# Kernel tuning notes

Measured on AMD Instinct MI355X. Metric: run time of the kernel, lower is better.

The kernel has to match this reference:

```python
import jax, jax.numpy as jnp
import numpy as np

B, N, H = 32, 1024, 512
THR = 0.05  # peak_detection_threshold


def _l2norm(x):
    return x / jnp.linalg.norm(x, axis=-1, keepdims=True)


def setup_inputs() -> dict:
    key = jax.random.key(0)
    ks = jax.random.split(key, 6)
    def w(k, shape, fan_in):
        return jax.random.normal(k, shape, jnp.float32) / np.float32(np.sqrt(fan_in))
    return {
        "segment_rep": jax.random.normal(ks[0], (B, N, H), jnp.float32),
        "phn_mask": jnp.ones((B, N), jnp.float32),
        # SegmentSimilarityMeasure: Linear(2H->H), ReLU, Linear(H->1, no bias)
        "W1": w(ks[1], (2 * H, H), 2 * H),
        "b1": jnp.zeros((H,), jnp.float32),
        "W2": w(ks[2], (H, 1), H),
        # word_enc: Linear(H->H), ReLU, Linear(H->H)
        "We1": w(ks[3], (H, H), H),
        "be1": jnp.zeros((H,), jnp.float32),
        "We2": w(ks[4], (H, H), H),
        "be2": jnp.zeros((H,), jnp.float32),
    }


def _forward(segment_rep, phn_mask, W1, b1, W2, We1, be1, We2, be2):
    Bs, Np, Hd = segment_rep.shape
    # adjacent segment similarity: MLP on concat of l2-normalized neighbors -> (B, N-1)
    cat = jnp.concatenate([_l2norm(segment_rep[:, :-1, :]), _l2norm(segment_rep[:, 1:, :])], axis=2)
    S = (jax.nn.relu(cat @ W1 + b1) @ W2)[..., 0]

    # relative dissimilarity
    Smin = jnp.min(S, axis=1, keepdims=True)
    Smax = jnp.max(S, axis=1, keepdims=True)
    D = 1.0 - (S - Smin) / (Smax - Smin)

    # peak detector (faithful to original, incl. final overwrite of first-order cols -2:)
    z = jnp.zeros_like(D)
    fo = z
    fo = fo.at[:, 0].set(jnp.maximum(D[:, 0] - D[:, 1], 0.0))
    fo = fo.at[:, 1:-1].set(jnp.minimum(jnp.maximum(D[:, 1:-1] - D[:, :-2], 0.0),
                                        jnp.maximum(D[:, 1:-1] - D[:, 2:], 0.0)))
    fo = fo.at[:, -1].set(jnp.maximum(D[:, -1] - D[:, -2], 0.0))
    so = z
    so = so.at[:, 0:2].set(jnp.maximum(D[:, 0:2] - D[:, 2:4], 0.0))
    so = so.at[:, 2:-2].set(jnp.minimum(jnp.maximum(D[:, 2:-2] - D[:, :-4], 0.0),
                                        jnp.maximum(D[:, 2:-2] - D[:, 4:], 0.0)))
    fo = fo.at[:, -2:].set(jnp.maximum(D[:, -2:] - D[:, -4:-2], 0.0))  # replicates original code
    P = jnp.minimum(jnp.maximum(jnp.maximum(fo, so) - THR, 0.0), fo)

    # pad, mask, straight-through hard boundaries
    P = jnp.pad(P, ((0, 0), (0, 1)))
    P = jax.nn.relu(P + (phn_mask - 1.0))
    b_soft = jnp.tanh(10.0 * P)
    b_hard = jnp.tanh(100000.0 * P)
    b = b_soft + jax.lax.stop_gradient(b_hard - b_soft)
    b = jnp.cumsum(b, axis=1)  # (B, N)
    b = b + (b[:, :1] == 0).astype(b.dtype)  # per-row +1 if b[:,0]==0
    num_word_segments = b[:, -1].astype(jnp.int32) + 1  # (B,)

    # U: column j holds j+1 for j < num_word_segments[i], else -100000. Nmax = N (static bound).
    cols = jnp.arange(1, Np + 1, dtype=jnp.int32)  # (Nmax,)
    U = jnp.where(cols[None, :] <= num_word_segments[:, None],
                  cols.astype(segment_rep.dtype)[None, :], -100000.0)  # (B, Nmax)

    V = U[:, None, :] - b[:, :, None]  # (B, N, Nmax)
    Wseg = 1.0 - jnp.tanh(100000.0 * jnp.abs(V))
    Wseg = Wseg / jnp.sum(Wseg, axis=1, keepdims=True)
    Wseg = jnp.nan_to_num(Wseg)

    # pool: (B, Nmax, N) @ (B, N, H) -> (B, Nmax, H)
    word_rep = jnp.einsum('bnm,bnh->bmh', Wseg, segment_rep)
    word_masks = jnp.where(word_rep == 0, 0.0, 1.0)
    out = jax.nn.relu(word_rep @ We1 + be1) @ We2 + be2
    return out * word_masks


def reference(segment_rep, phn_mask, W1, b1, W2, We1, be1, We2, be2):
    return _forward(segment_rep, phn_mask, W1, b1, W2, We1, be1, We2, be2)
```

## Files before the change

kernel.cpp:

```cpp
#include <hip/hip_runtime.h>

#define BB 32
#define NN 1024
#define HH 512
#define NS 1023

typedef unsigned short u16;
typedef unsigned int   u32;
typedef __attribute__((ext_vector_type(8))) short bf16x8;
typedef __attribute__((ext_vector_type(4))) float f32x4;

__device__ __forceinline__ float bf2f(u16 h) {
  union { u32 u; float f; } c; c.u = ((u32)h) << 16; return c.f;
}
__device__ __forceinline__ u16 f2bf(float f) {
  union { float f; u32 u; } c; c.f = f;
  u32 u = c.u;
  return (u16)((u + 0x7fffu + ((u >> 16) & 1u)) >> 16);
}
__device__ __forceinline__ void split_bf(float x, u16& hi, u16& lo) {
  hi = f2bf(x);
  lo = f2bf(x - bf2f(hi));
}
__device__ __forceinline__ void dma16(const u16* g, u16* l) {
  __builtin_amdgcn_global_load_lds(
      (const __attribute__((address_space(1))) u32*)g,
      (__attribute__((address_space(3))) u32*)l, 16, 0, 0);
}

__global__ __launch_bounds__(64) void k_prep_a(const float* __restrict__ seg,
                                               u16* __restrict__ ahi,
                                               u16* __restrict__ alo) {
  int row = blockIdx.x, lane = threadIdx.x;
  const float4* p = (const float4*)(seg + ((size_t)row << 9) + lane * 8);
  float4 a = p[0], b = p[1];
  float v[8] = {a.x, a.y, a.z, a.w, b.x, b.y, b.z, b.w};
  float s = 0.f;
#pragma unroll
  for (int i = 0; i < 8; ++i) s += v[i] * v[i];
#pragma unroll
  for (int m = 32; m; m >>= 1) s += __shfl_xor(s, m, 64);
  float nrm = sqrtf(s);
  u16 h[8], l[8];
#pragma unroll
  for (int i = 0; i < 8; ++i) split_bf(v[i] / nrm, h[i], l[i]);
  size_t off = ((size_t)row << 9) + lane * 8;
  *(uint4*)(ahi + off) = make_uint4(h[0] | (h[1] << 16), h[2] | (h[3] << 16),
                                    h[4] | (h[5] << 16), h[6] | (h[7] << 16));
  *(uint4*)(alo + off) = make_uint4(l[0] | (l[1] << 16), l[2] | (l[3] << 16),
                                    l[4] | (l[5] << 16), l[6] | (l[7] << 16));
}

__global__ __launch_bounds__(256) void k_tr(const float* __restrict__ src,
                                            u16* __restrict__ dh,
                                            u16* __restrict__ dl,
                                            int K, int N) {
  __shared__ u16 Th[64 * 66], Tl[64 * 66];
  int nb = blockIdx.x * 64, kb = blockIdx.y * 64;
  int tid = threadIdx.x;
#pragma unroll
  for (int i = 0; i < 16; ++i) {
    int e = tid + i * 256;
    int r = e >> 6, c = e & 63;
    float v = src[(size_t)(kb + r) * N + nb + c];
    u16 hi, lo; split_bf(v, hi, lo);
    Th[c * 66 + r] = hi;
    Tl[c * 66 + r] = lo;
  }
  __syncthreads();
#pragma unroll
  for (int i = 0; i < 16; ++i) {
    int e = tid + i * 256;
    int n = e >> 6, k = e & 63;
    dh[(size_t)(nb + n) * K + kb + k] = Th[n * 66 + k];
    if (dl) dl[(size_t)(nb + n) * K + kb + k] = Tl[n * 66 + k];
  }
}

__global__ __launch_bounds__(512, 2) void k_sgemm(const u16* __restrict__ ahi,
                                                  const u16* __restrict__ alo,
                                                  const u16* __restrict__ w1h,
                                                  const u16* __restrict__ w1l,
                                                  const float* __restrict__ b1,
                                                  const float* __restrict__ W2,
                                                  float* __restrict__ Spart) {
  __shared__ u16 Ah[2][256 * 32];
  __shared__ u16 Al[2][256 * 32];
  __shared__ u16 Bh[2][256 * 32];
  __shared__ u16 Bl[2][256 * 32];

  const int tid  = threadIdx.x;
  const int wave = tid >> 6, lane = tid & 63;
  const int quad = lane >> 4, l15 = lane & 15;
  const int wm = wave >> 2, wn = wave & 3;
  const int r_in = lane >> 2, c_in = lane & 3;
  const int nblk = blockIdx.x, mblk = blockIdx.y;
  const int mrow0 = mblk * 256;
  const int ncol0 = nblk * 256;

#define SG_A(g_, tb_, ks_)                                                   \
  {                                                                          \
    int k0_ = (ks_) * 32, half_ = k0_ >> 9, cb_ = k0_ & 511;                 \
    int grow_ = mrow0 + wave * 32 + (g_) * 16 + r_in + half_;                \
    if (grow_ > 32767) grow_ = 32767;                                        \
    size_t ga_ = (((size_t)grow_) << 9) + cb_ + c_in * 8;                    \
    dma16(ahi + ga_, &Ah[tb_][(wave * 32 + (g_) * 16) * 32]);                \
    dma16(alo + ga_, &Al[tb_][(wave * 32 + (g_) * 16) * 32]);                \
  }
#define SG_B(g_, tb_, ks_)                                                   \
  {                                                                          \
    int k0_ = (ks_) * 32;                                                    \
    int n_ = ncol0 + wave * 32 + (g_) * 16 + r_in;                           \
    size_t gb_ = (((size_t)n_) << 10) + k0_ + c_in * 8;                      \
    dma16(w1h + gb_, &Bh[tb_][(wave * 32 + (g_) * 16) * 32]);                \
    dma16(w1l + gb_, &Bl[tb_][(wave * 32 + (g_) * 16) * 32]);                \
  }

  f32x4 acc[8][4];
#pragma unroll
  for (int mi = 0; mi < 8; ++mi)
#pragma unroll
    for (int ni = 0; ni < 4; ++ni) acc[mi][ni] = (f32x4){0.f, 0.f, 0.f, 0.f};

  SG_A(0, 0, 0) SG_A(1, 0, 0) SG_B(0, 0, 0) SG_B(1, 0, 0)
  asm volatile("s_waitcnt vmcnt(0)" ::: "memory");
  __builtin_amdgcn_s_barrier();

  for (int ks = 0; ks < 32; ++ks) {
    const int bb = ks & 1;
    const bool pre = (ks + 1) < 32;
    bf16x8 ah[8], al[8], bh[4], bl[4];

#pragma unroll
    for (int mi = 0; mi < 8; ++mi)
      ah[mi] = *(const bf16x8*)&Ah[bb][(wm * 128 + mi * 16 + l15) * 32 + quad * 8];
#pragma unroll
    for (int ni = 0; ni < 4; ++ni)
      bh[ni] = *(const bf16x8*)&Bh[bb][(wn * 64 + ni * 16 + l15) * 32 + quad * 8];
    if (pre) { SG_A(0, bb ^ 1, ks + 1) SG_B(0, bb ^ 1, ks + 1) }
    __builtin_amdgcn_s_barrier();
    asm volatile("s_waitcnt lgkmcnt(0)" ::: "memory");
    __builtin_amdgcn_sched_barrier(0);
    __builtin_amdgcn_s_setprio(1);
#pragma unroll
    for (int ni = 0; ni < 4; ++ni)
#pragma unroll
      for (int mi = 0; mi < 8; ++mi)
        acc[mi][ni] = __builtin_amdgcn_mfma_f32_16x16x32_bf16(ah[mi], bh[ni], acc[mi][ni], 0, 0, 0);
    __builtin_amdgcn_s_setprio(0);
    __builtin_amdgcn_s_barrier();

#pragma unroll
    for (int ni = 0; ni < 4; ++ni)
      bl[ni] = *(const bf16x8*)&Bl[bb][(wn * 64 + ni * 16 + l15) * 32 + quad * 8];
    if (pre) { SG_A(1, bb ^ 1, ks + 1) SG_B(1, bb ^ 1, ks + 1) }
    __builtin_amdgcn_s_barrier();
    asm volatile("s_waitcnt lgkmcnt(0)" ::: "memory");
    __builtin_amdgcn_sched_barrier(0);
    __builtin_amdgcn_s_setprio(1);
#pragma unroll
    for (int ni = 0; ni < 4; ++ni)
#pragma unroll
      for (int mi = 0; mi < 8; ++mi)
        acc[mi][ni] = __builtin_amdgcn_mfma_f32_16x16x32_bf16(ah[mi], bl[ni], acc[mi][ni], 0, 0, 0);
    __builtin_amdgcn_s_setprio(0);
    __builtin_amdgcn_s_barrier();

#pragma unroll
    for (int mi = 0; mi < 8; ++mi)
      al[mi] = *(const bf16x8*)&Al[bb][(wm * 128 + mi * 16 + l15) * 32 + quad * 8];
    __builtin_amdgcn_s_barrier();
    asm volatile("s_waitcnt lgkmcnt(0)" ::: "memory");
    __builtin_amdgcn_sched_barrier(0);
    __builtin_amdgcn_s_setprio(1);
#pragma unroll
    for (int ni = 0; ni < 4; ++ni)
#pragma unroll
      for (int mi = 0; mi < 8; ++mi)
        acc[mi][ni] = __builtin_amdgcn_mfma_f32_16x16x32_bf16(al[mi], bh[ni], acc[mi][ni], 0, 0, 0);
    __builtin_amdgcn_s_setprio(0);
    asm volatile("s_waitcnt vmcnt(0)" ::: "memory");
    __builtin_amdgcn_s_barrier();
  }
#undef SG_A
#undef SG_B

  float* red = (float*)&Ah[0][0];
  float b1v[4], w2v[4];
#pragma unroll
  for (int ni = 0; ni < 4; ++ni) {
    int n_g = ncol0 + wn * 64 + ni * 16 + l15;
    b1v[ni] = b1[n_g];
    w2v[ni] = W2[n_g];
  }
#pragma unroll
  for (int mi = 0; mi < 8; ++mi) {
#pragma unroll
    for (int reg = 0; reg < 4; ++reg) {
      float part = 0.f;
#pragma unroll
      for (int ni = 0; ni < 4; ++ni) {
        float h = acc[mi][ni][reg] + b1v[ni];
        h = h > 0.f ? h : 0.f;
        part = fmaf(h, w2v[ni], part);
      }
#pragma unroll
      for (int m = 8; m; m >>= 1) part += __shfl_xor(part, m, 64);
      if (l15 == 0) red[wave * 128 + mi * 16 + quad * 4 + reg] = part;
    }
  }
  __syncthreads();
  if (tid < 256) {
    int wmr = tid >> 7, rl = tid & 127;
    float s = red[(wmr * 4 + 0) * 128 + rl] + red[(wmr * 4 + 1) * 128 + rl]
            + red[(wmr * 4 + 2) * 128 + rl] + red[(wmr * 4 + 3) * 128 + rl];
    int grow = mrow0 + tid;
    int b = grow >> 10, n = grow & 1023;
    if (n < NS)
      Spart[((size_t)nblk * BB + b) * NN + n] = s;
  }
}

__global__ __launch_bounds__(256) void k_row(const float* __restrict__ S0,
                                             const float* __restrict__ S1,
                                             const float* __restrict__ mask,
                                             int* __restrict__ assign,
                                             float* __restrict__ weight,
                                             float* __restrict__ total,
                                             int* __restrict__ startn,
                                             int* __restrict__ endn) {
  int b = blockIdx.x, tid = threadIdx.x;
  __shared__ float Ssh[NS];
  __shared__ float Dsh[NS];
  __shared__ float tsh[NN];
  __shared__ float bsh[NN];
  __shared__ float totl[NN];
  __shared__ int   stl[NN];
  __shared__ int   enl[NN];
  __shared__ float red[256];

  for (int n = tid; n < NS; n += 256)
    Ssh[n] = S0[((size_t)b << 10) + n] + S1[((size_t)b << 10) + n];
  __syncthreads();

  float mn = INFINITY, mx = -INFINITY;
  for (int n = tid; n < NS; n += 256) {
    float v = Ssh[n];
    mn = fminf(mn, v); mx = fmaxf(mx, v);
  }
  red[tid] = mn; __syncthreads();
  for (int s = 128; s; s >>= 1) { if (tid < s) red[tid] = fminf(red[tid], red[tid + s]); __syncthreads(); }
  float Smin = red[0]; __syncthreads();
  red[tid] = mx; __syncthreads();
  for (int s = 128; s; s >>= 1) { if (tid < s) red[tid] = fmaxf(red[tid], red[tid + s]); __syncthreads(); }
  float Smax = red[0]; __syncthreads();

  for (int n = tid; n < NS; n += 256)
    Dsh[n] = 1.0f - (Ssh[n] - Smin) / (Smax - Smin);
  __syncthreads();

  for (int n = tid; n < NN; n += 256) {
    float P;
    if (n >= NS) {
      P = 0.f;
    } else {
      float D = Dsh[n];
      float fo, so;
      if (n == 0)            fo = fmaxf(D - Dsh[1], 0.f);
      else if (n >= NS - 2)  fo = fmaxf(D - Dsh[n - 2], 0.f);
      else                   fo = fminf(fmaxf(D - Dsh[n - 1], 0.f),
                                        fmaxf(D - Dsh[n + 1], 0.f));
      if (n <= 1)            so = fmaxf(D - Dsh[n + 2], 0.f);
      else if (n >= NS - 2)  so = 0.f;
      else                   so = fminf(fmaxf(D - Dsh[n - 2], 0.f),
                                        fmaxf(D - Dsh[n + 2], 0.f));
      P = fminf(fmaxf(fmaxf(fo, so) - 0.05f, 0.f), fo);
    }
    float m = mask[((size_t)b << 10) + n];
    P = P + (m - 1.0f);
    P = P > 0.f ? P : 0.f;
    float bs = tanhf(10.0f * P);
    float bh = tanhf(100000.0f * P);
    tsh[n] = bs + (bh - bs);
  }
  __syncthreads();

  if (tid == 0) {
    float acc = 0.f;
    for (int n = 0; n < NN; n += 8) {
      float t0 = tsh[n + 0], t1 = tsh[n + 1], t2 = tsh[n + 2], t3 = tsh[n + 3];
      float t4 = tsh[n + 4], t5 = tsh[n + 5], t6 = tsh[n + 6], t7 = tsh[n + 7];
      acc += t0; bsh[n + 0] = acc; acc += t1; bsh[n + 1] = acc;
      acc += t2; bsh[n + 2] = acc; acc += t3; bsh[n + 3] = acc;
      acc += t4; bsh[n + 4] = acc; acc += t5; bsh[n + 5] = acc;
      acc += t6; bsh[n + 6] = acc; acc += t7; bsh[n + 7] = acc;
    }
  }
  __syncthreads();

  float add1 = (bsh[0] == 0.0f) ? 1.0f : 0.0f;
  int   num  = (int)(bsh[NN - 1] + add1) + 1;

  for (int mi = tid; mi < NN; mi += 256) { totl[mi] = 0.f; stl[mi] = 1 << 30; enl[mi] = -1; }
  __syncthreads();

  for (int n = tid; n < NN; n += 256) {
    float bv = bsh[n] + add1;
    float kf = rintf(bv);
    int   k  = (int)kf;
    int   a  = -1; float w = 0.f;
    if (k >= 1 && k <= num && k <= NN) {
      float v = fabsf(kf - bv);
      w = 1.0f - tanhf(100000.0f * v);
      if (w > 0.f) {
        a = k - 1;
        atomicAdd(&totl[a], w);
        atomicMin(&stl[a], n);
        atomicMax(&enl[a], n);
      } else {
        a = -1; w = 0.f;
      }
    }
    assign[((size_t)b << 10) + n] = a;
    weight[((size_t)b << 10) + n] = w;
  }
  __syncthreads();
  for (int mi = tid; mi < NN; mi += 256) {
    total [((size_t)b << 10) + mi] = totl[mi];
    startn[((size_t)b << 10) + mi] = stl[mi];
    endn  [((size_t)b << 10) + mi] = enl[mi];
  }
}

__global__ __launch_bounds__(64) void k_pool(const float* __restrict__ seg,
                                             const int* __restrict__ assign,
                                             const float* __restrict__ weight,
                                             const float* __restrict__ total,
                                             const int* __restrict__ startn,
                                             const int* __restrict__ endn,
                                             float* __restrict__ wrep) {
  int bm = blockIdx.x;
  int b  = bm >> 10, m = bm & 1023;
  int lane = threadIdx.x;
  float acc[8] = {0.f, 0.f, 0.f, 0.f, 0.f, 0.f, 0.f, 0.f};
  float tm = total[bm];
  if (tm > 0.f) {
    int s = startn[bm], e = endn[bm];
    for (int n = s; n <= e; ++n) {
      if (assign[((size_t)b << 10) + n] != m) continue;
      float coef = weight[((size_t)b << 10) + n] / tm;
      const float4* p = (const float4*)(seg + (((size_t)b << 10) + n) * HH + lane * 8);
      float4 x = p[0], y = p[1];
      acc[0] = fmaf(coef, x.x, acc[0]); acc[1] = fmaf(coef, x.y, acc[1]);
      acc[2] = fmaf(coef, x.z, acc[2]); acc[3] = fmaf(coef, x.w, acc[3]);
      acc[4] = fmaf(coef, y.x, acc[4]); acc[5] = fmaf(coef, y.y, acc[5]);
      acc[6] = fmaf(coef, y.z, acc[6]); acc[7] = fmaf(coef, y.w, acc[7]);
    }
  }
  float4* dst = (float4*)(wrep + (size_t)bm * HH + lane * 8);
  dst[0] = make_float4(acc[0], acc[1], acc[2], acc[3]);
  dst[1] = make_float4(acc[4], acc[5], acc[6], acc[7]);
}

__global__ __launch_bounds__(512) void k_out(const u16* __restrict__ we1t,
                                             const u16* __restrict__ we2t,
                                             const float* __restrict__ be1,
                                             const float* __restrict__ be2,
                                             float* __restrict__ io) {
  __shared__ u16 Hid[64 * 520];
  __shared__ u16 Wst[2][512 * 32];
  __shared__ u16 Ast[2][64 * 32];

  int tid = threadIdx.x;
  int wave = tid >> 6, lane = tid & 63, quad = lane >> 4, l15 = lane & 15;
  int wm = wave >> 2, wn = wave & 3;
  int rowbase = blockIdx.x * 64;
  int m_st = tid >> 3, ch_st = tid & 7;
  int r_in = lane >> 2, c_in = lane & 3;

#define STAGE_W(src_, ks_, tb_)                                                     \
  {                                                                                 \
    int k0_ = (ks_) * 32;                                                           \
    _Pragma("unroll")                                                               \
    for (int c_ = 0; c_ < 4; ++c_) {                                                \
      int n_ = wave * 64 + c_ * 16 + r_in;                                          \
      dma16(src_ + (size_t)n_ * 512 + k0_ + c_in * 8,                               \
            &Wst[tb_][(wave * 64 + c_ * 16) * 32]);                                 \
    }                                                                               \
  }

  f32x4 acc[2][8];
#pragma unroll
  for (int mi = 0; mi < 2; ++mi)
#pragma unroll
    for (int ni = 0; ni < 8; ++ni) acc[mi][ni] = (f32x4){0.f, 0.f, 0.f, 0.f};

  {
    float4 v = *(const float4*)(io + (size_t)(rowbase + m_st) * HH + ch_st * 4);
    u32 p0 = f2bf(v.x) | ((u32)f2bf(v.y) << 16);
    u32 p1 = f2bf(v.z) | ((u32)f2bf(v.w) << 16);
    *(uint2*)&Ast[0][m_st * 32 + ch_st * 4] = make_uint2(p0, p1);
  }
  STAGE_W(we1t, 0, 0)
  __syncthreads();

  for (int ks = 0; ks < 16; ++ks) {
    int bb = ks & 1;
    bool have = (ks + 1) < 16;
    float4 nx;
    if (have) {
      STAGE_W(we1t, ks + 1, bb ^ 1)
      nx = *(const float4*)(io + (size_t)(rowbase + m_st) * HH + (ks + 1) * 32 + ch_st * 4);
    }
    bf16x8 a[2];
#pragma unroll
    for (int mi = 0; mi < 2; ++mi)
      a[mi] = *(const bf16x8*)&Ast[bb][(wm * 32 + mi * 16 + l15) * 32 + quad * 8];
#pragma unroll
    for (int ni = 0; ni < 8; ++ni) {
      bf16x8 bw = *(const bf16x8*)&Wst[bb][(wn * 128 + ni * 16 + l15) * 32 + quad * 8];
#pragma unroll
      for (int mi = 0; mi < 2; ++mi)
        acc[mi][ni] = __builtin_amdgcn_mfma_f32_16x16x32_bf16(a[mi], bw, acc[mi][ni], 0, 0, 0);
    }
    if (have) {
      u32 p0 = f2bf(nx.x) | ((u32)f2bf(nx.y) << 16);
      u32 p1 = f2bf(nx.z) | ((u32)f2bf(nx.w) << 16);
      *(uint2*)&Ast[bb ^ 1][m_st * 32 + ch_st * 4] = make_uint2(p0, p1);
    }
    __syncthreads();
  }
#pragma unroll
  for (int mi = 0; mi < 2; ++mi)
#pragma unroll
    for (int ni = 0; ni < 8; ++ni)
#pragma unroll
      for (int reg = 0; reg < 4; ++reg) {
        int n_g = wn * 128 + ni * 16 + l15;
        float h = acc[mi][ni][reg] + be1[n_g];
        h = h > 0.f ? h : 0.f;
        Hid[(wm * 32 + mi * 16 + quad * 4 + reg) * 520 + n_g] = f2bf(h);
      }

#pragma unroll
  for (int mi = 0; mi < 2; ++mi)
#pragma unroll
    for (int ni = 0; ni < 8; ++ni) acc[mi][ni] = (f32x4){0.f, 0.f, 0.f, 0.f};

  STAGE_W(we2t, 0, 0)
  __syncthreads();

  for (int ks = 0; ks < 16; ++ks) {
    int bb = ks & 1;
    if (ks + 1 < 16) STAGE_W(we2t, ks + 1, bb ^ 1)
    int k0 = ks * 32;
    bf16x8 a[2];
#pragma unroll
    for (int mi = 0; mi < 2; ++mi)
      a[mi] = *(const bf16x8*)&Hid[(wm * 32 + mi * 16 + l15) * 520 + k0 + quad * 8];
#pragma unroll
    for (int ni = 0; ni < 8; ++ni) {
      bf16x8 bw = *(const bf16x8*)&Wst[bb][(wn * 128 + ni * 16 + l15) * 32 + quad * 8];
#pragma unroll
      for (int mi = 0; mi < 2; ++mi)
        acc[mi][ni] = __builtin_amdgcn_mfma_f32_16x16x32_bf16(a[mi], bw, acc[mi][ni], 0, 0, 0);
    }
    __syncthreads();
  }
#undef STAGE_W

#pragma unroll
  for (int mi = 0; mi < 2; ++mi)
#pragma unroll
    for (int ni = 0; ni < 8; ++ni)
#pragma unroll
      for (int reg = 0; reg < 4; ++reg) {
        int n_g = wn * 128 + ni * 16 + l15;
        size_t row = (size_t)(rowbase + wm * 32 + mi * 16 + quad * 4 + reg);
        float o = acc[mi][ni][reg] + be2[n_g];
        float wr = io[row * HH + n_g];
        io[row * HH + n_g] = (wr == 0.f) ? 0.f : o;
      }
}

__global__ void k_diag(float* __restrict__ out, int hostcode) {
  if (hostcode != 0) out[0] = (float)hostcode;
}

extern "C" void kernel_launch(void* const* d_in, const int* in_sizes, int n_in,
                              void* d_out, int out_size, void* d_ws, size_t ws_size,
                              hipStream_t stream) {
  const float* seg  = (const float*)d_in[0];
  const float* mask = (const float*)d_in[1];
  const float* W1   = (const float*)d_in[2];
  const float* b1   = (const float*)d_in[3];
  const float* W2   = (const float*)d_in[4];
  const float* We1  = (const float*)d_in[5];
  const float* be1  = (const float*)d_in[6];
  const float* We2  = (const float*)d_in[7];
  const float* be2  = (const float*)d_in[8];

  const size_t NROW = (size_t)BB * NN;
  float* ws = (float*)d_ws;
  float* S0     = ws;
  float* S1     = S0 + NROW;
  int*   assign = (int*)(S1 + NROW);
  float* weight = (float*)(assign + NROW);
  float* total  = weight + NROW;
  int*   startn = (int*)(total + NROW);
  int*   endn   = startn + NROW;
  u16*   w1h    = (u16*)(endn + NROW);
  u16*   w1l    = w1h + (size_t)512 * 1024;
  u16*   we1t   = w1l + (size_t)512 * 1024;
  u16*   we2t   = we1t + (size_t)512 * 512;

  float* out = (float*)d_out;
  u16*   ahi = (u16*)d_out;
  u16*   alo = ahi + (size_t)NROW * HH;

  int hostcode = 0;
  if (ws_size < (size_t)7 * NROW * 4 + (size_t)3 * 1024 * 1024) hostcode += 32768;
  if (out_size != 16777216) hostcode += 8192;

  k_prep_a<<<dim3(BB * NN), dim3(64), 0, stream>>>(seg, ahi, alo);
  k_tr    <<<dim3(8, 16), dim3(256), 0, stream>>>(W1, w1h, w1l, 1024, 512);
  k_tr    <<<dim3(8, 8),  dim3(256), 0, stream>>>(We1, we1t, (u16*)nullptr, 512, 512);
  k_tr    <<<dim3(8, 8),  dim3(256), 0, stream>>>(We2, we2t, (u16*)nullptr, 512, 512);
  k_sgemm <<<dim3(2, 128), dim3(512), 0, stream>>>(ahi, alo, w1h, w1l, b1, W2, S0);
  k_row   <<<dim3(BB), dim3(256), 0, stream>>>(S0, S1, mask, assign, weight, total, startn, endn);
  k_pool  <<<dim3(BB * NN), dim3(64), 0, stream>>>(seg, assign, weight, total, startn, endn, out);
  k_out   <<<dim3(NROW / 64), dim3(512), 0, stream>>>(we1t, we2t, be1, be2, out);
  k_diag  <<<dim3(1), dim3(1), 0, stream>>>(out, hostcode);
}
```

Baseline: 353.5 us.

## Split word encoder into two bf16 GEMM launches with packed zero-mask

The pooling kernel now writes word representations as bf16 plus a per-element zero bitmask, instead of fp32 values that are later reread. The fused two-stage encoder kernel is replaced by one generic GEMM kernel, launched twice. The first launch writes the ReLU hidden layer to global memory as bf16, in the upper half of each row's buffer. The second launch reads it back, and its epilogue applies the bitmask instead of reloading fp32 inputs. Both operands are staged by direct DMA with explicit waitcnt/barrier and raised priority around the MFMA block. This cuts the fp32 traffic and the in-loop conversion, but adds a global round trip for the hidden activations and an extra launch, and reuses the output buffer in place.

```diff
diff --git a/kernel.cpp b/kernel.cpp
--- a/kernel.cpp
+++ b/kernel.cpp
@@ -338,7 +338,8 @@
                                              const float* __restrict__ total,
                                              const int* __restrict__ startn,
                                              const int* __restrict__ endn,
-                                             float* __restrict__ wrep) {
+                                             u16* hrep,
+                                             unsigned char* __restrict__ mb) {
   int bm = blockIdx.x;
   int b  = bm >> 10, m = bm & 1023;
   int lane = threadIdx.x;
@@ -357,36 +358,50 @@
       acc[6] = fmaf(coef, y.z, acc[6]); acc[7] = fmaf(coef, y.w, acc[7]);
     }
   }
-  float4* dst = (float4*)(wrep + (size_t)bm * HH + lane * 8);
-  dst[0] = make_float4(acc[0], acc[1], acc[2], acc[3]);
-  dst[1] = make_float4(acc[4], acc[5], acc[6], acc[7]);
-}
-
-__global__ __launch_bounds__(512) void k_out(const u16* __restrict__ we1t,
-                                             const u16* __restrict__ we2t,
-                                             const float* __restrict__ be1,
-                                             const float* __restrict__ be2,
-                                             float* __restrict__ io) {
-  __shared__ u16 Hid[64 * 520];
-  __shared__ u16 Wst[2][512 * 32];
-  __shared__ u16 Ast[2][64 * 32];
-
-  int tid = threadIdx.x;
-  int wave = tid >> 6, lane = tid & 63, quad = lane >> 4, l15 = lane & 15;
-  int wm = wave >> 2, wn = wave & 3;
-  int rowbase = blockIdx.x * 64;
-  int m_st = tid >> 3, ch_st = tid & 7;
-  int r_in = lane >> 2, c_in = lane & 3;
-
-#define STAGE_W(src_, ks_, tb_)                                                     \
-  {                                                                                 \
-    int k0_ = (ks_) * 32;                                                           \
-    _Pragma("unroll")                                                               \
-    for (int c_ = 0; c_ < 4; ++c_) {                                                \
-      int n_ = wave * 64 + c_ * 16 + r_in;                                          \
-      dma16(src_ + (size_t)n_ * 512 + k0_ + c_in * 8,                               \
-            &Wst[tb_][(wave * 64 + c_ * 16) * 32]);                                 \
-    }                                                                               \
+  u16 h[8];
+  unsigned int mbyte = 0;
+#pragma unroll
+  for (int j = 0; j < 8; ++j) {
+    h[j] = f2bf(acc[j]);
+    mbyte |= (acc[j] == 0.f ? 1u : 0u) << j;
+  }
+  *(uint4*)(hrep + ((size_t)bm << 10) + lane * 8) =
+      make_uint4(h[0] | (h[1] << 16), h[2] | (h[3] << 16),
+                 h[4] | (h[5] << 16), h[6] | (h[7] << 16));
+  mb[((size_t)bm << 6) + lane] = (unsigned char)mbyte;
+}
+
+__global__ __launch_bounds__(512, 4) void k_g(const u16* asrc,
+                                              const u16* __restrict__ bmat,
+                                              const float* __restrict__ bias,
+                                              const unsigned char* __restrict__ mb,
+                                              float* outp,
+                                              u16* hid,
+                                              int a_off, int mode) {
+  __shared__ u16 As[2][64 * 32];
+  __shared__ u16 Bs[2][512 * 32];
+
+  const int tid  = threadIdx.x;
+  const int wave = tid >> 6, lane = tid & 63;
+  const int quad = lane >> 4, l15 = lane & 15;
+  const int wm = wave >> 2, wn = wave & 3;
+  const int r_in = lane >> 2, c_in = lane & 3;
+  const int mrow0 = blockIdx.x * 64;
+
+#define SG(tb_, ks_)                                                         \
+  {                                                                          \
+    int k0_ = (ks_) * 32;                                                    \
+    if (wave < 4) {                                                          \
+      int row_ = wave * 16 + r_in;                                           \
+      dma16(asrc + ((size_t)(mrow0 + row_) << 10) + a_off + k0_ + c_in * 8,  \
+            &As[tb_][(wave * 16) * 32]);                                     \
+    }                                                                        \
+    _Pragma("unroll")                                                        \
+    for (int g_ = 0; g_ < 4; ++g_) {                                         \
+      int n_ = wave * 64 + g_ * 16 + r_in;                                   \
+      dma16(bmat + (size_t)n_ * 512 + k0_ + c_in * 8,                        \
+            &Bs[tb_][(wave * 64 + g_ * 16) * 32]);                           \
+    }                                                                        \
   }
 
   f32x4 acc[2][8];
@@ -395,92 +410,65 @@
 #pragma unroll
     for (int ni = 0; ni < 8; ++ni) acc[mi][ni] = (f32x4){0.f, 0.f, 0.f, 0.f};
 
-  {
-    float4 v = *(const float4*)(io + (size_t)(rowbase + m_st) * HH + ch_st * 4);
-    u32 p0 = f2bf(v.x) | ((u32)f2bf(v.y) << 16);
-    u32 p1 = f2bf(v.z) | ((u32)f2bf(v.w) << 16);
-    *(uint2*)&Ast[0][m_st * 32 + ch_st * 4] = make_uint2(p0, p1);
-  }
-  STAGE_W(we1t, 0, 0)
-  __syncthreads();
+  SG(0, 0)
+  asm volatile("s_waitcnt vmcnt(0)" ::: "memory");
+  __builtin_amdgcn_s_barrier();
 
   for (int ks = 0; ks < 16; ++ks) {
-    int bb = ks & 1;
-    bool have = (ks + 1) < 16;
-    float4 nx;
-    if (have) {
-      STAGE_W(we1t, ks + 1, bb ^ 1)
-      nx = *(const float4*)(io + (size_t)(rowbase + m_st) * HH + (ks + 1) * 32 + ch_st * 4);
-    }
-    bf16x8 a[2];
+    const int bb = ks & 1;
+    bf16x8 a[2], b[8];
 #pragma unroll
     for (int mi = 0; mi < 2; ++mi)
-      a[mi] = *(const bf16x8*)&Ast[bb][(wm * 32 + mi * 16 + l15) * 32 + quad * 8];
-#pragma unroll
-    for (int ni = 0; ni < 8; ++ni) {
-      bf16x8 bw = *(const bf16x8*)&Wst[bb][(wn * 128 + ni * 16 + l15) * 32 + quad * 8];
+      a[mi] = *(const bf16x8*)&As[bb][(wm * 32 + mi * 16 + l15) * 32 + quad * 8];
+#pragma unroll
+    for (int ni = 0; ni < 8; ++ni)
+      b[ni] = *(const bf16x8*)&Bs[bb][(wn * 128 + ni * 16 + l15) * 32 + quad * 8];
+    if (ks + 1 < 16) SG(bb ^ 1, ks + 1)
+    asm volatile("s_waitcnt lgkmcnt(0)" ::: "memory");
+    __builtin_amdgcn_sched_barrier(0);
+    __builtin_amdgcn_s_setprio(1);
+#pragma unroll
+    for (int ni = 0; ni < 8; ++ni)
 #pragma unroll
       for (int mi = 0; mi < 2; ++mi)
-        acc[mi][ni] = __builtin_amdgcn_mfma_f32_16x16x32_bf16(a[mi], bw, acc[mi][ni], 0, 0, 0);
-    }
-    if (have) {
-      u32 p0 = f2bf(nx.x) | ((u32)f2bf(nx.y) << 16);
-      u32 p1 = f2bf(nx.z) | ((u32)f2bf(nx.w) << 16);
-      *(uint2*)&Ast[bb ^ 1][m_st * 32 + ch_st * 4] = make_uint2(p0, p1);
-    }
-    __syncthreads();
-  }
-#pragma unroll
-  for (int mi = 0; mi < 2; ++mi)
-#pragma unroll
-    for (int ni = 0; ni < 8; ++ni)
-#pragma unroll
-      for (int reg = 0; reg < 4; ++reg) {
-        int n_g = wn * 128 + ni * 16 + l15;
-        float h = acc[mi][ni][reg] + be1[n_g];
-        h = h > 0.f ? h : 0.f;
-        Hid[(wm * 32 + mi * 16 + quad * 4 + reg) * 520 + n_g] = f2bf(h);
-      }
-
-#pragma unroll
-  for (int mi = 0; mi < 2; ++mi)
-#pragma unroll
-    for (int ni = 0; ni < 8; ++ni) acc[mi][ni] = (f32x4){0.f, 0.f, 0.f, 0.f};
-
-  STAGE_W(we2t, 0, 0)
-  __syncthreads();
-
-  for (int ks = 0; ks < 16; ++ks) {
-    int bb = ks & 1;
-    if (ks + 1 < 16) STAGE_W(we2t, ks + 1, bb ^ 1)
-    int k0 = ks * 32;
-    bf16x8 a[2];
+        acc[mi][ni] = __builtin_amdgcn_mfma_f32_16x16x32_bf16(a[mi], b[ni], acc[mi][ni], 0, 0, 0);
+    __builtin_amdgcn_s_setprio(0);
+    asm volatile("s_waitcnt vmcnt(0)" ::: "memory");
+    __builtin_amdgcn_s_barrier();
+  }
+#undef SG
+
+  float bv[8];
+#pragma unroll
+  for (int ni = 0; ni < 8; ++ni) bv[ni] = bias[wn * 128 + ni * 16 + l15];
+
+  if (mode == 1) {
 #pragma unroll
     for (int mi = 0; mi < 2; ++mi)
-      a[mi] = *(const bf16x8*)&Hid[(wm * 32 + mi * 16 + l15) * 520 + k0 + quad * 8];
-#pragma unroll
-    for (int ni = 0; ni < 8; ++ni) {
-      bf16x8 bw = *(const bf16x8*)&Wst[bb][(wn * 128 + ni * 16 + l15) * 32 + quad * 8];
-#pragma unroll
-      for (int mi = 0; mi < 2; ++mi)
-        acc[mi][ni] = __builtin_amdgcn_mfma_f32_16x16x32_bf16(a[mi], bw, acc[mi][ni], 0, 0, 0);
-    }
-    __syncthreads();
-  }
-#undef STAGE_W
-
-#pragma unroll
-  for (int mi = 0; mi < 2; ++mi)
-#pragma unroll
-    for (int ni = 0; ni < 8; ++ni)
-#pragma unroll
-      for (int reg = 0; reg < 4; ++reg) {
-        int n_g = wn * 128 + ni * 16 + l15;
-        size_t row = (size_t)(rowbase + wm * 32 + mi * 16 + quad * 4 + reg);
-        float o = acc[mi][ni][reg] + be2[n_g];
-        float wr = io[row * HH + n_g];
-        io[row * HH + n_g] = (wr == 0.f) ? 0.f : o;
-      }
+#pragma unroll
+      for (int ni = 0; ni < 8; ++ni)
+#pragma unroll
+        for (int reg = 0; reg < 4; ++reg) {
+          int col = wn * 128 + ni * 16 + l15;
+          int row = mrow0 + wm * 32 + mi * 16 + quad * 4 + reg;
+          float h = acc[mi][ni][reg] + bv[ni];
+          h = h > 0.f ? h : 0.f;
+          hid[((size_t)row << 10) + 512 + col] = f2bf(h);
+        }
+  } else {
+#pragma unroll
+    for (int mi = 0; mi < 2; ++mi)
+#pragma unroll
+      for (int ni = 0; ni < 8; ++ni)
+#pragma unroll
+        for (int reg = 0; reg < 4; ++reg) {
+          int col = wn * 128 + ni * 16 + l15;
+          int row = mrow0 + wm * 32 + mi * 16 + quad * 4 + reg;
+          float o = acc[mi][ni][reg] + bv[ni];
+          unsigned char m8 = mb[((size_t)row << 6) + (col >> 3)];
+          outp[((size_t)row << 9) + col] = ((m8 >> (col & 7)) & 1) ? 0.f : o;
+        }
+  }
 }
 
 __global__ void k_diag(float* __restrict__ out, int hostcode) {
@@ -517,6 +505,8 @@
   float* out = (float*)d_out;
   u16*   ahi = (u16*)d_out;
   u16*   alo = ahi + (size_t)NROW * HH;
+  u16*   hrep = (u16*)d_out;
+  unsigned char* mbuf = (unsigned char*)w1h;
 
   int hostcode = 0;
   if (ws_size < (size_t)7 * NROW * 4 + (size_t)3 * 1024 * 1024) hostcode += 32768;
@@ -528,7 +518,8 @@
   k_tr    <<<dim3(8, 8),  dim3(256), 0, stream>>>(We2, we2t, (u16*)nullptr, 512, 512);
   k_sgemm <<<dim3(2, 128), dim3(512), 0, stream>>>(ahi, alo, w1h, w1l, b1, W2, S0);
   k_row   <<<dim3(BB), dim3(256), 0, stream>>>(S0, S1, mask, assign, weight, total, startn, endn);
-  k_pool  <<<dim3(BB * NN), dim3(64), 0, stream>>>(seg, assign, weight, total, startn, endn, out);
-  k_out   <<<dim3(NROW / 64), dim3(512), 0, stream>>>(we1t, we2t, be1, be2, out);
+  k_pool  <<<dim3(BB * NN), dim3(64), 0, stream>>>(seg, assign, weight, total, startn, endn, hrep, mbuf);
+  k_g     <<<dim3(512), dim3(512), 0, stream>>>(hrep, we1t, be1, mbuf, out, hrep, 0,   1);
+  k_g     <<<dim3(512), dim3(512), 0, stream>>>(hrep, we2t, be2, mbuf, out, hrep, 512, 2);
   k_diag  <<<dim3(1), dim3(1), 0, stream>>>(out, hostcode);
 }
```

Result: faster. 325.5 us (-7.9%).
